# Kernel optimization log

Hardware: AMD Instinct MI355X
Metric: run time of the kernel (lower is better)

## Reference

```python
import jax, jax.numpy as jnp
import numpy as np

B, C, H, W = 8, 512, 48, 48
WSCALE = 0.02  # keep pre-softmax energies in a sane range


def _conv(x, w, b, stride, pad):
    y = jax.lax.conv_general_dilated(
        x, w, (stride, stride), [(pad, pad), (pad, pad)],
        dimension_numbers=("NCHW", "OIHW", "NCHW"))
    return y + b[None, :, None, None]


def setup_inputs() -> dict:
    key = jax.random.key(0)
    ks = jax.random.split(key, 9)
    return {
        "x": jax.random.normal(ks[0], (B, C, H, W), jnp.float32),
        "Wqc": jax.random.normal(ks[1], (2 * C, C, 3, 3), jnp.float32) * WSCALE,
        "bqc": jax.random.normal(ks[2], (2 * C,), jnp.float32) * WSCALE,
        "Wkc": jax.random.normal(ks[3], (C, C, 3, 3), jnp.float32) * WSCALE,
        "bkc": jax.random.normal(ks[4], (C,), jnp.float32) * WSCALE,
        "Wqp": jax.random.normal(ks[5], (C // 8, C, 1, 1), jnp.float32) * WSCALE,
        "bqp": jax.random.normal(ks[6], (C // 8,), jnp.float32) * WSCALE,
        "Wkp": jax.random.normal(ks[7], (C // 8, C, 1, 1), jnp.float32) * WSCALE,
        "bkp": jax.random.normal(ks[8], (C // 8,), jnp.float32) * WSCALE,
    }


def reference(x, Wqc, bqc, Wkc, bkc, Wqp, bqp, Wkp, bkp):
    b, c, h, w = x.shape
    hw = h * w
    # --- channel attention (CAM) on stride-2 downsampled q/k ---
    qc = _conv(x, Wqc, bqc, 2, 1).reshape(b, 2 * c, -1)   # (B, 2C, H'W')
    kc = _conv(x, Wkc, bkc, 2, 1).reshape(b, c, -1)       # (B, C,  H'W')
    energy = jnp.einsum("bqm,bcm->bqc", qc, kc)            # (B, 2C, C)
    # max-subtraction trick from the source: max - energy, then softmax
    energy_new = jnp.max(energy, axis=-1, keepdims=True) - energy
    attn_c = jax.nn.softmax(energy_new, axis=-1)
    xf = x.reshape(b, c, hw)
    out_c = jnp.einsum("bqc,bcn->bqn", attn_c, xf)         # (B, 2C, HW)
    # --- position attention (PAM) ---
    qp = _conv(x, Wqp, bqp, 1, 0).reshape(b, c // 8, hw)   # (B, C/8, HW)
    kp = _conv(x, Wkp, bkp, 1, 0).reshape(b, c // 8, hw)   # (B, C/8, HW)
    energy_p = jnp.einsum("bdn,bdm->bnm", qp, kp)          # (B, HW, HW)
    attn_p = jax.nn.softmax(energy_p, axis=-1)
    # out_c @ attn_p^T
    out_p = jnp.einsum("bqn,bmn->bqm", out_c, attn_p)      # (B, 2C, HW)
    return out_c, out_p.reshape(b, 2 * c, h, w)
```

## Files before the change

### kernel.cpp

```cpp
#include <hip/hip_runtime.h>
#include <hip/hip_bf16.h>

typedef unsigned short u16;
typedef __attribute__((ext_vector_type(8))) _Float16 half8;
typedef __attribute__((ext_vector_type(4))) float f32x4;

static __device__ __forceinline__ u16 f2h(float v) {
  return __builtin_bit_cast(u16, (_Float16)v);
}
static __device__ __forceinline__ float h2f(u16 u) {
  return (float)__builtin_bit_cast(_Float16, u);
}

static __device__ __forceinline__ void gll16(const void* g, void* l) {
  __builtin_amdgcn_global_load_lds(
      (const __attribute__((address_space(1))) unsigned int*)g,
      (__attribute__((address_space(3))) unsigned int*)l, 16, 0, 0);
}

template <int N>
static __device__ __forceinline__ void wait_vm() {
  if constexpr (N == 0) asm volatile("s_waitcnt vmcnt(0)" ::: "memory");
  else if constexpr (N == 4) asm volatile("s_waitcnt vmcnt(4)" ::: "memory");
  else if constexpr (N == 6) asm volatile("s_waitcnt vmcnt(6)" ::: "memory");
  else asm volatile("s_waitcnt vmcnt(8)" ::: "memory");
}

template <bool ASPLIT, bool BSPLIT, int EPI>
__global__ __launch_bounds__(256) void gemm_bt(
    const u16* __restrict__ A, const u16* __restrict__ Al,
    const u16* __restrict__ B, const u16* __restrict__ Bl,
    float* __restrict__ Cf, u16* __restrict__ Ch, u16* __restrict__ Cl,
    const float* __restrict__ bias0, const float* __restrict__ bias1,
    int biasSplit, int K, int lda, int ldb, int ldc,
    long long sA, long long sB, long long sC) {
  __shared__ __align__(16) u16 smA[3][(ASPLIT ? 2 : 1) * 128 * 32];
  __shared__ __align__(16) u16 smB[3][(BSPLIT ? 2 : 1) * 128 * 32];
  constexpr int G = 4 + (ASPLIT ? 2 : 0) + (BSPLIT ? 2 : 0);

  const int tid = threadIdx.x;
  const int wave = tid >> 6, lane = tid & 63;
  const int wr = wave >> 1, wc = wave & 1;

  const int gx = gridDim.x, gy = gridDim.y;
  const int nwg = gx * gy * (int)gridDim.z;
  const int bid = (int)blockIdx.x + gx * ((int)blockIdx.y + gy * (int)blockIdx.z);
  const int w = (bid & 7) * (nwg >> 3) + (bid >> 3);
  const int bx = w % gx;
  const int rem = w / gx;
  const int by = rem % gy;
  const long long z = rem / gy;

  A += z * sA;
  B += z * sB;
  if (ASPLIT) Al += z * sA;
  if (BSPLIT) Bl += z * sB;
  const long long tM = (long long)by * 128;
  const long long tN = (long long)bx * 128;
  const int r4 = lane >> 2, kc = lane & 3;

  const long long arow0 = (tM + wave * 16 + r4) * (long long)lda + kc * 8;
  const long long arow1 = arow0 + 64LL * lda;
  const long long brow0 = (tN + wave * 16 + r4) * (long long)ldb + kc * 8;
  const long long brow1 = brow0 + 64LL * ldb;

  auto stage = [&](int bf, long long ko) {
    u16* dA = &smA[bf][wave * 512];
    u16* dB = &smB[bf][wave * 512];
    gll16(A + arow0 + ko, dA);
    gll16(A + arow1 + ko, dA + 2048);
    gll16(B + brow0 + ko, dB);
    gll16(B + brow1 + ko, dB + 2048);
    if constexpr (ASPLIT) {
      gll16(Al + arow0 + ko, dA + 4096);
      gll16(Al + arow1 + ko, dA + 4096 + 2048);
    }
    if constexpr (BSPLIT) {
      gll16(Bl + brow0 + ko, dB + 4096);
      gll16(Bl + brow1 + ko, dB + 4096 + 2048);
    }
  };

  f32x4 acc[4][4];
#pragma unroll
  for (int i = 0; i < 4; i++)
#pragma unroll
    for (int j = 0; j < 4; j++) acc[i][j] = f32x4{0.f, 0.f, 0.f, 0.f};

  const int quad = lane >> 4, mr = lane & 15;
  const int nk = K >> 5;

  stage(0, 0);
  if (nk > 1) stage(1, 32);

  int cur = 0;
  for (int kt = 0; kt < nk; ++kt) {
    if (kt < nk - 1) wait_vm<G>(); else wait_vm<0>();
    __builtin_amdgcn_s_barrier();
    asm volatile("" ::: "memory");

    half8 a[4], b[4];
#pragma unroll
    for (int i = 0; i < 4; i++)
      a[i] = *(const half8*)&smA[cur][(wr * 64 + i * 16 + mr) * 32 + quad * 8];
#pragma unroll
    for (int j = 0; j < 4; j++)
      b[j] = *(const half8*)&smB[cur][(wc * 64 + j * 16 + mr) * 32 + quad * 8];

    if (kt + 2 < nk) {
      int pf = cur + 2; if (pf >= 3) pf -= 3;
      stage(pf, (long long)(kt + 2) * 32);
    }

#pragma unroll
    for (int i = 0; i < 4; i++)
#pragma unroll
      for (int j = 0; j < 4; j++)
        acc[i][j] = __builtin_amdgcn_mfma_f32_16x16x32_f16(a[i], b[j], acc[i][j], 0, 0, 0);

    if constexpr (ASPLIT) {
      half8 al[4];
#pragma unroll
      for (int i = 0; i < 4; i++)
        al[i] = *(const half8*)&smA[cur][4096 + (wr * 64 + i * 16 + mr) * 32 + quad * 8];
#pragma unroll
      for (int i = 0; i < 4; i++)
#pragma unroll
        for (int j = 0; j < 4; j++)
          acc[i][j] = __builtin_amdgcn_mfma_f32_16x16x32_f16(al[i], b[j], acc[i][j], 0, 0, 0);
    }
    if constexpr (BSPLIT) {
      half8 bl[4];
#pragma unroll
      for (int j = 0; j < 4; j++)
        bl[j] = *(const half8*)&smB[cur][4096 + (wc * 64 + j * 16 + mr) * 32 + quad * 8];
#pragma unroll
      for (int i = 0; i < 4; i++)
#pragma unroll
        for (int j = 0; j < 4; j++)
          acc[i][j] = __builtin_amdgcn_mfma_f32_16x16x32_f16(a[i], bl[j], acc[i][j], 0, 0, 0);
    }
    cur = (cur == 2) ? 0 : cur + 1;
  }

#pragma unroll
  for (int i = 0; i < 4; i++) {
#pragma unroll
    for (int j = 0; j < 4; j++) {
      const long long gn = tN + wc * 64 + j * 16 + mr;
#pragma unroll
      for (int p = 0; p < 4; p++) {
        const long long gm = tM + wr * 64 + i * 16 + quad * 4 + p;
        float v = acc[i][j][p];
        if constexpr (EPI == 1) v += (gm < biasSplit) ? bias0[gm] : bias1[gm - biasSplit];
        if constexpr (EPI == 3) v += (gn < biasSplit) ? bias0[gn] : bias1[gn - biasSplit];
        const long long off = z * sC + gm * ldc + gn;
        if constexpr (EPI == 0) {
          Cf[off] = v;
        } else if constexpr (EPI == 1) {
          u16 h = f2h(v);
          Ch[off] = h;
          Cl[off] = f2h(v - h2f(h));
        } else if constexpr (EPI == 2) {
          Cf[off] = v;
          Ch[off] = f2h(v);
        } else {
          Ch[off] = f2h(v);
        }
      }
    }
  }
  (void)biasSplit;
}

__global__ void im2col_kernel(const float* __restrict__ x, u16* __restrict__ Ph) {
  int idx = blockIdx.x * 256 + threadIdx.x;
  int k = idx % 4608;
  int m = idx / 4608;
  int kx = k % 3, t = k / 3;
  int ky = t % 3, c = t / 3;
  int ox = m % 24, t2 = m / 24;
  int oy = t2 % 24, b = t2 / 24;
  int ix = 2 * ox - 1 + kx, iy = 2 * oy - 1 + ky;
  float v = 0.f;
  if (ix >= 0 && ix < 48 && iy >= 0 && iy < 48)
    v = x[((b * 512 + c) * 48 + iy) * 48 + ix];
  Ph[idx] = f2h(v);
}

__global__ void wprep_kernel(const float* __restrict__ Wqc, const float* __restrict__ Wkc,
                             u16* __restrict__ Wh, u16* __restrict__ Wl) {
  int idx = blockIdx.x * 256 + threadIdx.x;
  int n = idx / 4608;
  float v = (n < 1024) ? Wqc[idx] : Wkc[idx - 1024 * 4608];
  u16 h = f2h(v);
  Wh[idx] = h;
  Wl[idx] = f2h(v - h2f(h));
}

__global__ void wp_prep(const float* __restrict__ Wqp, const float* __restrict__ Wkp,
                        u16* __restrict__ Wp) {
  int idx = blockIdx.x * 256 + threadIdx.x;
  int d = idx >> 9;
  float v = (d < 64) ? Wqp[idx] : Wkp[idx - 64 * 512];
  Wp[idx] = f2h(v);
}

__global__ void xt_kernel(const float* __restrict__ x, u16* __restrict__ xt) {
  __shared__ float t[32][33];
  int b = blockIdx.z;
  int sp0 = blockIdx.x * 32, c0 = blockIdx.y * 32;
  int tx = threadIdx.x & 31, ty = threadIdx.x >> 5;
#pragma unroll
  for (int k = 0; k < 4; k++) {
    int c = c0 + ty + k * 8;
    t[ty + k * 8][tx] = x[((long long)(b * 512 + c)) * 2304 + sp0 + tx];
  }
  __syncthreads();
#pragma unroll
  for (int k = 0; k < 4; k++) {
    int sp = sp0 + ty + k * 8;
    xt[((long long)b * 2304 + sp) * 512 + c0 + tx] = f2h(t[tx][ty + k * 8]);
  }
}

__global__ void softmax_cam(const float* __restrict__ E, u16* __restrict__ attn) {
  __shared__ float sm[4];
  const long long r = blockIdx.x;
  const float* e = E + r * 512;
  int tid = threadIdx.x, wave = tid >> 6, lane = tid & 63;
  float v0 = e[tid], v1 = e[tid + 256];
  float mn = fminf(v0, v1);
#pragma unroll
  for (int o = 32; o; o >>= 1) mn = fminf(mn, __shfl_xor(mn, o));
  if (lane == 0) sm[wave] = mn;
  __syncthreads();
  mn = fminf(fminf(sm[0], sm[1]), fminf(sm[2], sm[3]));
  float p0 = __expf(mn - v0), p1 = __expf(mn - v1);
  float s = p0 + p1;
#pragma unroll
  for (int o = 32; o; o >>= 1) s += __shfl_xor(s, o);
  __syncthreads();
  if (lane == 0) sm[wave] = s;
  __syncthreads();
  float inv = 1.f / (sm[0] + sm[1] + sm[2] + sm[3]);
  attn[r * 512 + tid] = f2h(p0 * inv);
  attn[r * 512 + tid + 256] = f2h(p1 * inv);
}

__global__ void softmax_pam(u16* __restrict__ EP) {
  __shared__ float sm[4];
  const long long r = blockIdx.x;
  u16* e = EP + r * 2304;
  int tid = threadIdx.x, wave = tid >> 6, lane = tid & 63;
  float v[9];
#pragma unroll
  for (int k = 0; k < 9; k++) v[k] = h2f(e[tid + 256 * k]);
  float mx = v[0];
#pragma unroll
  for (int k = 1; k < 9; k++) mx = fmaxf(mx, v[k]);
#pragma unroll
  for (int o = 32; o; o >>= 1) mx = fmaxf(mx, __shfl_xor(mx, o));
  if (lane == 0) sm[wave] = mx;
  __syncthreads();
  mx = fmaxf(fmaxf(sm[0], sm[1]), fmaxf(sm[2], sm[3]));
  float s = 0.f;
#pragma unroll
  for (int k = 0; k < 9; k++) {
    v[k] = __expf(v[k] - mx);
    s += v[k];
  }
#pragma unroll
  for (int o = 32; o; o >>= 1) s += __shfl_xor(s, o);
  __syncthreads();
  if (lane == 0) sm[wave] = s;
  __syncthreads();
  float inv = 1.f / (sm[0] + sm[1] + sm[2] + sm[3]);
#pragma unroll
  for (int k = 0; k < 9; k++) e[tid + 256 * k] = f2h(v[k] * inv);
}

extern "C" void kernel_launch(void* const* d_in, const int* in_sizes, int n_in,
                              void* d_out, int out_size, void* d_ws, size_t ws_size,
                              hipStream_t stream) {
  const float* x   = (const float*)d_in[0];
  const float* Wqc = (const float*)d_in[1];
  const float* bqc = (const float*)d_in[2];
  const float* Wkc = (const float*)d_in[3];
  const float* bkc = (const float*)d_in[4];
  const float* Wqp = (const float*)d_in[5];
  const float* bqp = (const float*)d_in[6];
  const float* Wkp = (const float*)d_in[7];
  const float* bkp = (const float*)d_in[8];
  float* outc = (float*)d_out;
  float* outp = outc + 8LL * 1024 * 2304;

  if (ws_size < 195166208ULL) return;

  char* ws = (char*)d_ws;
  u16*   P    = (u16*)(ws + 0);
  u16*   Wh   = (u16*)(ws + 42467328LL);
  u16*   Wl   = (u16*)(ws + 56623104LL);
  u16*   EP   = (u16*)(ws + 0);
  u16*   qcth = (u16*)(ws + 84934656LL);
  u16*   qctl = (u16*)(ws + 99090432LL);
  u16*   pp   = (u16*)(ws + 84934656LL);
  float* E    = (float*)(ws + 113246208LL);
  u16*   attn = (u16*)(ws + 130023424LL);
  u16*   xt   = (u16*)(ws + 138412032LL);
  u16*   ocb  = (u16*)(ws + 157286400LL);
  u16*   Wp   = (u16*)(ws + 195035136LL);

  wprep_kernel<<<27648, 256, 0, stream>>>(Wqc, Wkc, Wh, Wl);
  wp_prep<<<256, 256, 0, stream>>>(Wqp, Wkp, Wp);
  im2col_kernel<<<82944, 256, 0, stream>>>(x, P);
  xt_kernel<<<dim3(72, 16, 8), 256, 0, stream>>>(x, xt);

  gemm_bt<true, false, 1><<<dim3(36, 12, 1), 256, 0, stream>>>(
      Wh, Wl, P, nullptr, nullptr, qcth, qctl, bqc, bkc, 1024,
      4608, 4608, 4608, 4608, 0, 0, 0);

  gemm_bt<true, true, 0><<<dim3(4, 8, 8), 256, 0, stream>>>(
      qcth, qctl, qcth + 1024LL * 4608, qctl + 1024LL * 4608,
      E, nullptr, nullptr,
      nullptr, nullptr, 0, 576, 4608, 4608, 512, 576, 576, 524288);

  softmax_cam<<<8192, 256, 0, stream>>>(E, attn);

  gemm_bt<false, false, 2><<<dim3(18, 8, 8), 256, 0, stream>>>(
      attn, nullptr, xt, nullptr, outc, ocb, nullptr,
      nullptr, nullptr, 0, 512, 512, 512, 2304, 524288, 1179648, 2359296);

  gemm_bt<false, false, 3><<<dim3(1, 144, 1), 256, 0, stream>>>(
      xt, nullptr, Wp, nullptr, nullptr, pp, nullptr,
      bqp, bkp, 64, 512, 512, 512, 128, 0, 0, 0);

  gemm_bt<false, false, 4><<<dim3(18, 18, 8), 256, 0, stream>>>(
      pp, nullptr, pp + 64, nullptr, nullptr, EP, nullptr,
      nullptr, nullptr, 0, 64, 128, 128, 2304, 294912, 294912, 5308416);

  softmax_pam<<<18432, 256, 0, stream>>>(EP);

  gemm_bt<false, false, 0><<<dim3(18, 8, 8), 256, 0, stream>>>(
      ocb, nullptr, EP, nullptr, outp, nullptr, nullptr,
      nullptr, nullptr, 0, 2304, 2304, 2304, 2304, 2359296, 5308416, 2359296);

  (void)in_sizes; (void)n_in; (void)out_size;
}
```

Baseline: 674.2 us.

## Vectorize prep kernels and PAM softmax to 16-byte accesses, simplify 2D block mapping

The im2col and weight-prep kernels now have each thread produce 8 consecutive fp16 values and write them with one 16-byte store, and their launch grids shrink by 8x to match. The PAM softmax reads and writes each 2304-element row as 8-wide vectors, with a tail handled by the first 32 threads. The GEMM skips the XCD-swizzled block remapping when gridDim.z is 1 and uses blockIdx directly. Together these aim to cut memory-instruction count and index arithmetic in the bandwidth-bound prep and softmax stages. The trade-offs are less cache-friendly block placement for single-batch GEMMs and uncoalesced strided gathers in im2col.

```diff
diff --git a/kernel.cpp b/kernel.cpp
--- a/kernel.cpp
+++ b/kernel.cpp
@@ -3,6 +3,7 @@
 
 typedef unsigned short u16;
 typedef __attribute__((ext_vector_type(8))) _Float16 half8;
+typedef __attribute__((ext_vector_type(8))) unsigned short u16x8;
 typedef __attribute__((ext_vector_type(4))) float f32x4;
 
 static __device__ __forceinline__ u16 f2h(float v) {
@@ -43,13 +44,21 @@
   const int wr = wave >> 1, wc = wave & 1;
 
   const int gx = gridDim.x, gy = gridDim.y;
-  const int nwg = gx * gy * (int)gridDim.z;
-  const int bid = (int)blockIdx.x + gx * ((int)blockIdx.y + gy * (int)blockIdx.z);
-  const int w = (bid & 7) * (nwg >> 3) + (bid >> 3);
-  const int bx = w % gx;
-  const int rem = w / gx;
-  const int by = rem % gy;
-  const long long z = rem / gy;
+  int bx, by;
+  long long z;
+  if (gridDim.z > 1) {
+    const int nwg = gx * gy * (int)gridDim.z;
+    const int bid = (int)blockIdx.x + gx * ((int)blockIdx.y + gy * (int)blockIdx.z);
+    const int w = (bid & 7) * (nwg >> 3) + (bid >> 3);
+    bx = w % gx;
+    const int rem = w / gx;
+    by = rem % gy;
+    z = rem / gy;
+  } else {
+    bx = blockIdx.x;
+    by = blockIdx.y;
+    z = 0;
+  }
 
   A += z * sA;
   B += z * sB;
@@ -175,27 +184,42 @@
 
 __global__ void im2col_kernel(const float* __restrict__ x, u16* __restrict__ Ph) {
   int idx = blockIdx.x * 256 + threadIdx.x;
-  int k = idx % 4608;
-  int m = idx / 4608;
-  int kx = k % 3, t = k / 3;
-  int ky = t % 3, c = t / 3;
+  int m = idx / 576;
+  int k0 = (idx - m * 576) * 8;
   int ox = m % 24, t2 = m / 24;
   int oy = t2 % 24, b = t2 / 24;
-  int ix = 2 * ox - 1 + kx, iy = 2 * oy - 1 + ky;
-  float v = 0.f;
-  if (ix >= 0 && ix < 48 && iy >= 0 && iy < 48)
-    v = x[((b * 512 + c) * 48 + iy) * 48 + ix];
-  Ph[idx] = f2h(v);
+  int iy_base = 2 * oy - 1, ix_base = 2 * ox - 1;
+  u16x8 out;
+#pragma unroll
+  for (int j = 0; j < 8; j++) {
+    int k = k0 + j;
+    int kx = k % 3, t = k / 3;
+    int ky = t % 3, c = t / 3;
+    int ix = ix_base + kx, iy = iy_base + ky;
+    float v = 0.f;
+    if (ix >= 0 && ix < 48 && iy >= 0 && iy < 48)
+      v = x[((b * 512 + c) * 48 + iy) * 48 + ix];
+    out[j] = f2h(v);
+  }
+  *(u16x8*)&Ph[(long long)idx * 8] = out;
 }
 
 __global__ void wprep_kernel(const float* __restrict__ Wqc, const float* __restrict__ Wkc,
                              u16* __restrict__ Wh, u16* __restrict__ Wl) {
   int idx = blockIdx.x * 256 + threadIdx.x;
-  int n = idx / 4608;
-  float v = (n < 1024) ? Wqc[idx] : Wkc[idx - 1024 * 4608];
-  u16 h = f2h(v);
-  Wh[idx] = h;
-  Wl[idx] = f2h(v - h2f(h));
+  long long base = (long long)idx * 8;
+  int n = idx / 576;
+  const float* src = (n < 1024) ? &Wqc[base] : &Wkc[base - 1024LL * 4608];
+  u16x8 h8, l8;
+#pragma unroll
+  for (int j = 0; j < 8; j++) {
+    float v = src[j];
+    u16 h = f2h(v);
+    h8[j] = h;
+    l8[j] = f2h(v - h2f(h));
+  }
+  *(u16x8*)&Wh[base] = h8;
+  *(u16x8*)&Wl[base] = l8;
 }
 
 __global__ void wp_prep(const float* __restrict__ Wqp, const float* __restrict__ Wkp,
@@ -253,12 +277,24 @@
   const long long r = blockIdx.x;
   u16* e = EP + r * 2304;
   int tid = threadIdx.x, wave = tid >> 6, lane = tid & 63;
-  float v[9];
-#pragma unroll
-  for (int k = 0; k < 9; k++) v[k] = h2f(e[tid + 256 * k]);
-  float mx = v[0];
-#pragma unroll
-  for (int k = 1; k < 9; k++) mx = fmaxf(mx, v[k]);
+  u16x8 m8 = *(const u16x8*)&e[tid * 8];
+  const bool hasTail = tid < 32;
+  u16x8 t8;
+  if (hasTail) t8 = *(const u16x8*)&e[2048 + tid * 8];
+  float v[8], w[8];
+  float mx = -1e30f;
+#pragma unroll
+  for (int k = 0; k < 8; k++) {
+    v[k] = h2f(m8[k]);
+    mx = fmaxf(mx, v[k]);
+  }
+  if (hasTail) {
+#pragma unroll
+    for (int k = 0; k < 8; k++) {
+      w[k] = h2f(t8[k]);
+      mx = fmaxf(mx, w[k]);
+    }
+  }
 #pragma unroll
   for (int o = 32; o; o >>= 1) mx = fmaxf(mx, __shfl_xor(mx, o));
   if (lane == 0) sm[wave] = mx;
@@ -266,10 +302,17 @@
   mx = fmaxf(fmaxf(sm[0], sm[1]), fmaxf(sm[2], sm[3]));
   float s = 0.f;
 #pragma unroll
-  for (int k = 0; k < 9; k++) {
+  for (int k = 0; k < 8; k++) {
     v[k] = __expf(v[k] - mx);
     s += v[k];
   }
+  if (hasTail) {
+#pragma unroll
+    for (int k = 0; k < 8; k++) {
+      w[k] = __expf(w[k] - mx);
+      s += w[k];
+    }
+  }
 #pragma unroll
   for (int o = 32; o; o >>= 1) s += __shfl_xor(s, o);
   __syncthreads();
@@ -277,7 +320,13 @@
   __syncthreads();
   float inv = 1.f / (sm[0] + sm[1] + sm[2] + sm[3]);
 #pragma unroll
-  for (int k = 0; k < 9; k++) e[tid + 256 * k] = f2h(v[k] * inv);
+  for (int k = 0; k < 8; k++) m8[k] = f2h(v[k] * inv);
+  *(u16x8*)&e[tid * 8] = m8;
+  if (hasTail) {
+#pragma unroll
+    for (int k = 0; k < 8; k++) t8[k] = f2h(w[k] * inv);
+    *(u16x8*)&e[2048 + tid * 8] = t8;
+  }
 }
 
 extern "C" void kernel_launch(void* const* d_in, const int* in_sizes, int n_in,
@@ -311,9 +360,9 @@
   u16*   ocb  = (u16*)(ws + 157286400LL);
   u16*   Wp   = (u16*)(ws + 195035136LL);
 
-  wprep_kernel<<<27648, 256, 0, stream>>>(Wqc, Wkc, Wh, Wl);
+  wprep_kernel<<<3456, 256, 0, stream>>>(Wqc, Wkc, Wh, Wl);
   wp_prep<<<256, 256, 0, stream>>>(Wqp, Wkp, Wp);
-  im2col_kernel<<<82944, 256, 0, stream>>>(x, P);
+  im2col_kernel<<<10368, 256, 0, stream>>>(x, P);
   xt_kernel<<<dim3(72, 16, 8), 256, 0, stream>>>(x, xt);
 
   gemm_bt<true, false, 1><<<dim3(36, 12, 1), 256, 0, stream>>>(
```

Result: slower. 716.3 us (+6.2%).
